# Performance work log

Measured on AMD Instinct MI355X. Metric: run time of the kernel, lower is better.

Reference implementation:

```python
import jax, jax.numpy as jnp
import numpy as np

N, KLEN, Q, S, E, H = 8, 512, 16, 128, 256, 8


def setup_inputs() -> dict:
    key = jax.random.key(0)
    ks = jax.random.split(key, 9)
    values = jax.random.normal(ks[0], (N, KLEN, E), dtype=jnp.float32)
    keys = jax.random.normal(ks[1], (N, KLEN, E), dtype=jnp.float32)
    query = jax.random.normal(ks[2], (N, Q, S, E), dtype=jnp.float32)
    mask = jax.random.randint(ks[3], (N, 1, 1, KLEN, 1), 0, 2, dtype=jnp.int32)
    Wv = jax.random.normal(ks[4], (E, E), dtype=jnp.float32) * 0.02
    Wk = jax.random.normal(ks[5], (E, E), dtype=jnp.float32) * 0.02
    Wq = jax.random.normal(ks[6], (E, E), dtype=jnp.float32) * 0.02
    Wo = jax.random.normal(ks[7], (E, H * E), dtype=jnp.float32) * 0.02
    bo = jnp.zeros((E,), dtype=jnp.float32)
    return {"values": values, "keys": keys, "query": query, "mask": mask,
            "Wv": Wv, "Wk": Wk, "Wq": Wq, "Wo": Wo, "bo": bo}


def reference(values, keys, query, mask, Wv, Wk, Wq, Wo, bo):
    # In the torch module head_dim == embed_size and the SAME Linear is applied
    # to every (expanded) head, so project once and broadcast over heads.
    e = Wq.shape[0]
    heads = Wo.shape[1] // e
    v = values @ Wv.T          # [N, K, E]
    k = keys @ Wk.T            # [N, K, E]
    q = query @ Wq.T           # [N, Q, S, E]
    # energy per head is identical; broadcast to [N, H, Q, K, S] to mirror
    # torch's einsum('nqshd,nkhd->nhqks') followed by masked_fill.
    energy = jnp.einsum('nqsd,nkd->nqks', q, k)               # [N, Q, K, S]
    energy = jnp.broadcast_to(energy[:, None],
                              (energy.shape[0], heads) + energy.shape[1:])
    energy = jnp.where(mask == 0, jnp.float32(-1e20), energy)  # [N,H,Q,K,S]
    attn = jax.nn.softmax(energy / jnp.sqrt(jnp.float32(e)), axis=3)
    out = jnp.einsum('nhqks,nkd->nqshd', attn, v)              # [N,Q,S,H,E]
    out = out.reshape(out.shape[0], out.shape[1], out.shape[2], heads * e)
    return out @ Wo.T + bo                                     # [N, Q, S, E]
```

## Files before the change

### kernel.cpp

```cpp
#include <hip/hip_runtime.h>
#include <hip/hip_bf16.h>
#include <stdint.h>

#define NB   8
#define KL   512
#define QD   16
#define SD   128
#define ED   256
#define RPN  (QD*SD)
#define BMR  32
#define FRAG 512
#define PAN  131072

typedef __hip_bfloat16 bf16;
using s16x8 = __attribute__((ext_vector_type(8))) short;
using f32x4 = __attribute__((ext_vector_type(4))) float;

__device__ __forceinline__ float b2f(unsigned short u){
    union { uint32_t i; float f; } v; v.i = ((uint32_t)u) << 16; return v.f;
}
__device__ __forceinline__ unsigned short f2b(float f){
    union { float ff; uint32_t i; } v; v.ff = f;
    uint32_t lsb = (v.i >> 16) & 1;
    v.i += 0x7FFFu + lsb;
    return (unsigned short)(v.i >> 16);
}
__device__ __forceinline__ uint32_t cvtpk(float lo, float hi){
    uint32_t r;
    asm("v_cvt_pk_bf16_f32 %0, %1, %2" : "=v"(r) : "v"(lo), "v"(hi));
    return r;
}
__device__ __forceinline__ f32x4 mfma16(s16x8 a, s16x8 b, f32x4 c){
    return __builtin_amdgcn_mfma_f32_16x16x32_bf16(a, b, c, 0, 0, 0);
}

template<bool B>
__device__ __forceinline__ float ldin(const void* p, size_t i){
    if (B) return b2f(((const unsigned short*)p)[i]);
    else   return ((const float*)p)[i];
}

__device__ bool probe_bf16(const uint32_t* __restrict__ w, int* pc){
    if (threadIdx.x == 0) *pc = 0;
    __syncthreads();
    if (threadIdx.x < 256){
        int local = 0;
        #pragma unroll
        for (int i = 0; i < 4; ++i){
            uint32_t x = w[threadIdx.x*4 + i];
            uint32_t e = (x >> 7) & 0xFFu;
            local += (e >= 120u && e <= 132u) ? 1 : 0;
        }
        if (local) atomicAdd(pc, local);
    }
    __syncthreads();
    return *pc > 512;
}

template<bool B>
__device__ void gt_body(const void* __restrict__ Wq, const void* __restrict__ Wk,
                        float* __restrict__ Gt, int bx){
    int b = bx, a = threadIdx.x;
    float s = 0.f;
    #pragma unroll 8
    for (int d = 0; d < 256; ++d)
        s += ldin<B>(Wq, (size_t)d*256 + a) * ldin<B>(Wk, (size_t)d*256 + b);
    Gt[b*256 + a] = s;
}
template<bool B>
__device__ void wosmt_body(const void* __restrict__ Wo, const void* __restrict__ Wv,
                           float* __restrict__ Mt, int bx, float (*sm)[256]){
    int t = threadIdx.x, e0 = bx*8;
    #pragma unroll
    for (int je = 0; je < 8; ++je){
        int e = e0 + je;
        float s = 0.f;
        #pragma unroll
        for (int h = 0; h < 8; ++h) s += ldin<B>(Wo, (size_t)e*2048 + h*256 + t);
        sm[je][t] = s;
    }
    __syncthreads();
    float acc[8] = {0,0,0,0,0,0,0,0};
    #pragma unroll 4
    for (int dp = 0; dp < 256; ++dp){
        float wv = ldin<B>(Wv, (size_t)dp*256 + t);
        #pragma unroll
        for (int je = 0; je < 8; ++je) acc[je] += sm[je][dp] * wv;
    }
    #pragma unroll
    for (int je = 0; je < 8; ++je) Mt[t*256 + e0 + je] = acc[je];
}
__global__ __launch_bounds__(256)
void k_prep(const void* __restrict__ values,
            const void* __restrict__ Wq, const void* __restrict__ Wk,
            const void* __restrict__ Wo, const void* __restrict__ Wv,
            float* __restrict__ Gt, float* __restrict__ Mt){
    __shared__ float sm[8][256];
    __shared__ int pc;
    bool bf = probe_bf16((const uint32_t*)values, &pc);
    if (blockIdx.x < 256){
        if (bf) gt_body<true >(Wq, Wk, Gt, blockIdx.x);
        else    gt_body<false>(Wq, Wk, Gt, blockIdx.x);
    } else {
        int bx = blockIdx.x - 256;
        if (bf) wosmt_body<true >(Wo, Wv, Mt, bx, sm);
        else    wosmt_body<false>(Wo, Wv, Mt, bx, sm);
    }
}

template<bool B>
__device__ void projK_body(const void* __restrict__ A, const float* __restrict__ Wt,
                           unsigned short* __restrict__ C, int bx, float (*As)[256]){
    int r0 = bx * 8;
    int t  = threadIdx.x;
    #pragma unroll
    for (int j = 0; j < 8; ++j)
        As[j][t] = ldin<B>(A, (size_t)(r0 + j)*256 + t);
    __syncthreads();
    float acc[8] = {0,0,0,0,0,0,0,0};
    #pragma unroll 4
    for (int i = 0; i < 256; ++i){
        float w = Wt[i*256 + t];
        #pragma unroll
        for (int j = 0; j < 8; ++j) acc[j] += As[j][i] * w;
    }
    int nn = r0 >> 9, key0 = r0 & 511;
    int K16 = key0 >> 4, ks = t >> 5, g = (t >> 3) & 3, i = t & 7;
    size_t base = (size_t)nn*PAN + (size_t)((K16*8 + ks)*64)*8;
    int l0 = (key0 & 15) | (g << 4);
    #pragma unroll
    for (int j = 0; j < 8; ++j)
        C[base + (size_t)(l0 + j)*8 + i] = f2b(acc[j]);
}
template<bool B>
__device__ void projU_body(const void* __restrict__ A, const float* __restrict__ Wt,
                           unsigned short* __restrict__ C, int bx, float (*As)[256]){
    int r0 = bx * 8;
    int t  = threadIdx.x;
    #pragma unroll
    for (int j = 0; j < 8; ++j)
        As[j][t] = ldin<B>(A, (size_t)(r0 + j)*256 + t);
    __syncthreads();
    float acc[8] = {0,0,0,0,0,0,0,0};
    #pragma unroll 4
    for (int i = 0; i < 256; ++i){
        float w = Wt[i*256 + t];
        #pragma unroll
        for (int j = 0; j < 8; ++j) acc[j] += As[j][i] * w;
    }
    int nn = r0 >> 9, k0 = r0 & 511;
    int ks2 = k0 >> 5, g = (k0 >> 3) & 3;
    int E16 = t >> 4, l = (t & 15) | (g << 4);
    size_t base = (size_t)nn*PAN + (size_t)((E16*16 + ks2)*64 + l)*8;
    union { s16x8 v; unsigned short h[8]; } pk;
    #pragma unroll
    for (int j = 0; j < 8; ++j) pk.h[j] = f2b(acc[j]);
    *(s16x8*)(&C[base]) = pk.v;
}
__global__ __launch_bounds__(256)
void k_proj2(const void* __restrict__ keys, const void* __restrict__ values,
             const float* __restrict__ Gt, const float* __restrict__ Mt,
             unsigned short* __restrict__ kkF, unsigned short* __restrict__ utF){
    __shared__ float As[8][256];
    __shared__ int pc;
    bool bf = probe_bf16((const uint32_t*)values, &pc);
    if (blockIdx.x < 512){
        if (bf) projK_body<true >(keys, Gt, kkF, blockIdx.x, As);
        else    projK_body<false>(keys, Gt, kkF, blockIdx.x, As);
    } else {
        int bx = blockIdx.x - 512;
        if (bf) projU_body<true >(values, Mt, utF, bx, As);
        else    projU_body<false>(values, Mt, utF, bx, As);
    }
}

template<bool B>
__device__ void fused_body(const void* __restrict__ query,
                           const unsigned short* __restrict__ kkF,
                           const unsigned short* __restrict__ utF,
                           const int* __restrict__ mask,
                           const void* __restrict__ bo,
                           void* __restrict__ out,
                           float* Sc, unsigned short* Qs){
    int bid = blockIdx.x;
    int n   = bid & 7;
    int r0  = (bid >> 3) * BMR;
    int t   = threadIdx.x;
    int l15 = t & 15;
    int g   = (t >> 4) & 3;
    int w   = t >> 6;
    int lane = t & 63;

    const unsigned short* Kn = kkF + (size_t)n*PAN;
    const unsigned short* Un = utF + (size_t)n*PAN;
    const int* mn = mask + n*KL;
    unsigned short* P = (unsigned short*)Sc;

    {
        int row = t >> 4;
        int c0  = (t & 15) * 16;
        int sw  = (row & 7) << 3;
        size_t qoff = (size_t)n*RPN*ED + (size_t)(r0 + row)*ED + c0;
        if (B){
            const unsigned short* qp = (const unsigned short*)query + qoff;
            s16x8 v0 = *(const s16x8*)(qp);
            s16x8 v1 = *(const s16x8*)(qp + 8);
            *(s16x8*)&Qs[(row*ED + c0    ) ^ sw] = v0;
            *(s16x8*)&Qs[(row*ED + c0 + 8) ^ sw] = v1;
        } else {
            const float* qp = (const float*)query + qoff;
            float4 x0 = *(const float4*)(qp);
            float4 x1 = *(const float4*)(qp + 4);
            float4 x2 = *(const float4*)(qp + 8);
            float4 x3 = *(const float4*)(qp + 12);
            union { s16x8 v; uint32_t u[4]; } pk;
            pk.u[0] = cvtpk(x0.x,x0.y); pk.u[1] = cvtpk(x0.z,x0.w);
            pk.u[2] = cvtpk(x1.x,x1.y); pk.u[3] = cvtpk(x1.z,x1.w);
            *(s16x8*)&Qs[(row*ED + c0    ) ^ sw] = pk.v;
            pk.u[0] = cvtpk(x2.x,x2.y); pk.u[1] = cvtpk(x2.z,x2.w);
            pk.u[2] = cvtpk(x3.x,x3.y); pk.u[3] = cvtpk(x3.z,x3.w);
            *(s16x8*)&Qs[(row*ED + c0 + 8) ^ sw] = pk.v;
        }
    }
    __syncthreads();

    int asw = (l15 & 7) << 3;

    {
        f32x4 acc1[2][4];
        #pragma unroll
        for (int rt = 0; rt < 2; ++rt)
            #pragma unroll
            for (int c = 0; c < 4; ++c) acc1[rt][c] = (f32x4){0.f,0.f,0.f,0.f};

        const unsigned short* kb = Kn + (size_t)w*16384 + (size_t)lane*8;
        s16x8 bb[3][4];
        auto LDK = [&](int KS, int SL){
            #pragma unroll
            for (int c = 0; c < 4; ++c)
                bb[SL][c] = *(const s16x8*)(kb + (size_t)(c*8 + KS)*FRAG);
        };
        LDK(0,0); LDK(1,1);
        #pragma unroll
        for (int ks = 0; ks < 8; ++ks){
            if (ks + 2 < 8) LDK(ks + 2, (ks + 2) % 3);
            int col = ks*32 + g*8;
            s16x8 a0 = *(const s16x8*)&Qs[(( 0 + l15)*ED + col) ^ asw];
            s16x8 a1 = *(const s16x8*)&Qs[((16 + l15)*ED + col) ^ asw];
            #pragma unroll
            for (int c = 0; c < 4; ++c){
                acc1[0][c] = mfma16(a0, bb[ks % 3][c], acc1[0][c]);
                acc1[1][c] = mfma16(a1, bb[ks % 3][c], acc1[1][c]);
            }
        }
        #pragma unroll
        for (int c = 0; c < 4; ++c){
            int key = w*64 + c*16 + l15;
            bool zz = (mn[key] == 0);
            #pragma unroll
            for (int rt = 0; rt < 2; ++rt){
                #pragma unroll
                for (int j = 0; j < 4; ++j){
                    int row = rt*16 + g*4 + j;
                    float v = zz ? -1e20f : acc1[rt][c][j] * 0.0625f;
                    Sc[(row*KL + key) ^ ((row & 7) << 2)] = v;
                }
            }
        }
    }
    __syncthreads();

    {
        int row = t >> 4, l16 = t & 15;
        int sw2 = (row & 7) << 2, sw3 = (row & 7) << 3;
        float xs[32];
        float m = -3.0e38f;
        #pragma unroll
        for (int i = 0; i < 32; ++i){
            xs[i] = Sc[(row*KL + l16 + 16*i) ^ sw2];
            m = fmaxf(m, xs[i]);
        }
        #pragma unroll
        for (int off = 1; off < 16; off <<= 1)
            m = fmaxf(m, __shfl_xor(m, off, 16));
        float s = 0.f;
        #pragma unroll
        for (int i = 0; i < 32; ++i){
            xs[i] = __expf(xs[i] - m);
            s += xs[i];
        }
        #pragma unroll
        for (int off = 1; off < 16; off <<= 1)
            s += __shfl_xor(s, off, 16);
        float inv = 1.0f / s;
        __syncthreads();
        #pragma unroll
        for (int i = 0; i < 32; ++i)
            P[(row*KL + l16 + 16*i) ^ sw3] = f2b(xs[i] * inv);
    }
    __syncthreads();

    {
        f32x4 acc2[2][2];
        #pragma unroll
        for (int rt = 0; rt < 2; ++rt)
            #pragma unroll
            for (int c = 0; c < 2; ++c) acc2[rt][c] = (f32x4){0.f,0.f,0.f,0.f};

        const unsigned short* ub = Un + (size_t)(2*w)*8192 + (size_t)lane*8;
        s16x8 bu[3][2];
        auto LDU = [&](int KS, int SL){
            #pragma unroll
            for (int c = 0; c < 2; ++c)
                bu[SL][c] = *(const s16x8*)(ub + (size_t)(c*16 + KS)*FRAG);
        };
        LDU(0,0); LDU(1,1);
        #pragma unroll
        for (int ks = 0; ks < 16; ++ks){
            if (ks + 2 < 16) LDU(ks + 2, (ks + 2) % 3);
            int col = ks*32 + g*8;
            s16x8 p0 = *(const s16x8*)&P[(( 0 + l15)*KL + col) ^ asw];
            s16x8 p1 = *(const s16x8*)&P[((16 + l15)*KL + col) ^ asw];
            #pragma unroll
            for (int c = 0; c < 2; ++c){
                acc2[0][c] = mfma16(p0, bu[ks % 3][c], acc2[0][c]);
                acc2[1][c] = mfma16(p1, bu[ks % 3][c], acc2[1][c]);
            }
        }
        float bov[2];
        #pragma unroll
        for (int c = 0; c < 2; ++c) bov[c] = ldin<B>(bo, (2*w + c)*16 + l15);
        #pragma unroll
        for (int rt = 0; rt < 2; ++rt){
            #pragma unroll
            for (int j = 0; j < 4; ++j){
                int row = rt*16 + g*4 + j;
                #pragma unroll
                for (int c = 0; c < 2; ++c){
                    int e = (2*w + c)*16 + l15;
                    float val = acc2[rt][c][j] + bov[c];
                    size_t oidx = (size_t)n*RPN*ED + (size_t)(r0 + row)*ED + e;
                    if (B) ((unsigned short*)out)[oidx] = f2b(val);
                    else   ((float*)out)[oidx] = val;
                }
            }
        }
    }
}

__global__ __launch_bounds__(512, 4)
void k_fused3(const void* __restrict__ values, const void* __restrict__ query,
              const unsigned short* __restrict__ kkF,
              const unsigned short* __restrict__ utF,
              const int* __restrict__ mask, const void* __restrict__ bo,
              void* __restrict__ out){
    __shared__ float Sc[BMR*KL];
    __shared__ unsigned short Qs[BMR*ED];
    bool bf = probe_bf16((const uint32_t*)values, (int*)Sc);
    if (bf) fused_body<true >(query, kkF, utF, mask, bo, out, Sc, Qs);
    else    fused_body<false>(query, kkF, utF, mask, bo, out, Sc, Qs);
}

extern "C" void kernel_launch(void* const* d_in, const int* in_sizes, int n_in,
                              void* d_out, int out_size, void* d_ws, size_t ws_size,
                              hipStream_t stream){
    const void* values = d_in[0];
    const void* keys   = d_in[1];
    const void* query  = d_in[2];
    const int*  mask   = (const int*)d_in[3];
    const void* Wv     = d_in[4];
    const void* Wk     = d_in[5];
    const void* Wq     = d_in[6];
    const void* Wo     = d_in[7];
    const void* bo     = d_in[8];

    float* ws = (float*)d_ws;
    float* ws_gt = ws;
    float* ws_mt = ws + 65536;
    unsigned short* ws_kk = (unsigned short*)(ws + 131072);
    unsigned short* ws_u  = ws_kk + (size_t)NB*PAN;

    k_prep  <<< 288, 256, 0, stream>>>(values, Wq, Wk, Wo, Wv, ws_gt, ws_mt);
    k_proj2 <<<1024, 256, 0, stream>>>(keys, values, ws_gt, ws_mt, ws_kk, ws_u);
    k_fused3<<< 512, 512, 0, stream>>>(values, query, ws_kk, ws_u, mask, bo, d_out);
}
```

Measured before the change: 150.5 us.

## Keep softmax scores in registers with cross-wave reductions and fragment-layout P

```diff
diff --git a/kernel.cpp b/kernel.cpp
--- a/kernel.cpp
+++ b/kernel.cpp
@@ -181,7 +181,8 @@
                            const int* __restrict__ mask,
                            const void* __restrict__ bo,
                            void* __restrict__ out,
-                           float* Sc, unsigned short* Qs){
+                           unsigned short* Qs, unsigned short* Pf,
+                           float* redM, float* redS){
     int bid = blockIdx.x;
     int n   = bid & 7;
     int r0  = (bid >> 3) * BMR;
@@ -194,7 +195,6 @@
     const unsigned short* Kn = kkF + (size_t)n*PAN;
     const unsigned short* Un = utF + (size_t)n*PAN;
     const int* mn = mask + n*KL;
-    unsigned short* P = (unsigned short*)Sc;
 
     {
         int row = t >> 4;
@@ -226,6 +226,7 @@
 
     int asw = (l15 & 7) << 3;
 
+    float p[2][4][4];
     {
         f32x4 acc1[2][4];
         #pragma unroll
@@ -255,48 +256,83 @@
         }
         #pragma unroll
         for (int c = 0; c < 4; ++c){
-            int key = w*64 + c*16 + l15;
-            bool zz = (mn[key] == 0);
-            #pragma unroll
-            for (int rt = 0; rt < 2; ++rt){
-                #pragma unroll
-                for (int j = 0; j < 4; ++j){
-                    int row = rt*16 + g*4 + j;
-                    float v = zz ? -1e20f : acc1[rt][c][j] * 0.0625f;
-                    Sc[(row*KL + key) ^ ((row & 7) << 2)] = v;
+            bool zz = (mn[w*64 + c*16 + l15] == 0);
+            #pragma unroll
+            for (int rt = 0; rt < 2; ++rt)
+                #pragma unroll
+                for (int j = 0; j < 4; ++j)
+                    p[rt][c][j] = zz ? -1e20f : acc1[rt][c][j] * 0.0625f;
+        }
+    }
+
+    {
+        float mx[2][4];
+        #pragma unroll
+        for (int rt = 0; rt < 2; ++rt)
+            #pragma unroll
+            for (int j = 0; j < 4; ++j){
+                float m0 = fmaxf(fmaxf(p[rt][0][j], p[rt][1][j]),
+                                 fmaxf(p[rt][2][j], p[rt][3][j]));
+                #pragma unroll
+                for (int off = 1; off < 16; off <<= 1)
+                    m0 = fmaxf(m0, __shfl_xor(m0, off, 16));
+                mx[rt][j] = m0;
+            }
+        if (l15 == 0){
+            #pragma unroll
+            for (int rt = 0; rt < 2; ++rt)
+                #pragma unroll
+                for (int j = 0; j < 4; ++j)
+                    redM[(rt*16 + g*4 + j)*8 + w] = mx[rt][j];
+        }
+        __syncthreads();
+        float sm[2][4];
+        #pragma unroll
+        for (int rt = 0; rt < 2; ++rt)
+            #pragma unroll
+            for (int j = 0; j < 4; ++j){
+                int row = rt*16 + g*4 + j;
+                float4 a = *(const float4*)&redM[row*8];
+                float4 b = *(const float4*)&redM[row*8 + 4];
+                float m = fmaxf(fmaxf(fmaxf(a.x,a.y),fmaxf(a.z,a.w)),
+                                fmaxf(fmaxf(b.x,b.y),fmaxf(b.z,b.w)));
+                float s = 0.f;
+                #pragma unroll
+                for (int c = 0; c < 4; ++c){
+                    p[rt][c][j] = __expf(p[rt][c][j] - m);
+                    s += p[rt][c][j];
                 }
-            }
-        }
-    }
-    __syncthreads();
-
-    {
-        int row = t >> 4, l16 = t & 15;
-        int sw2 = (row & 7) << 2, sw3 = (row & 7) << 3;
-        float xs[32];
-        float m = -3.0e38f;
-        #pragma unroll
-        for (int i = 0; i < 32; ++i){
-            xs[i] = Sc[(row*KL + l16 + 16*i) ^ sw2];
-            m = fmaxf(m, xs[i]);
-        }
-        #pragma unroll
-        for (int off = 1; off < 16; off <<= 1)
-            m = fmaxf(m, __shfl_xor(m, off, 16));
-        float s = 0.f;
-        #pragma unroll
-        for (int i = 0; i < 32; ++i){
-            xs[i] = __expf(xs[i] - m);
-            s += xs[i];
-        }
-        #pragma unroll
-        for (int off = 1; off < 16; off <<= 1)
-            s += __shfl_xor(s, off, 16);
-        float inv = 1.0f / s;
+                #pragma unroll
+                for (int off = 1; off < 16; off <<= 1)
+                    s += __shfl_xor(s, off, 16);
+                sm[rt][j] = s;
+            }
+        if (l15 == 0){
+            #pragma unroll
+            for (int rt = 0; rt < 2; ++rt)
+                #pragma unroll
+                for (int j = 0; j < 4; ++j)
+                    redS[(rt*16 + g*4 + j)*8 + w] = sm[rt][j];
+        }
         __syncthreads();
-        #pragma unroll
-        for (int i = 0; i < 32; ++i)
-            P[(row*KL + l16 + 16*i) ^ sw3] = f2b(xs[i] * inv);
+        int ihi = ((l15 >> 3) << 4);
+        int ilo = l15 & 7;
+        #pragma unroll
+        for (int rt = 0; rt < 2; ++rt){
+            #pragma unroll
+            for (int j = 0; j < 4; ++j){
+                int row = rt*16 + g*4 + j;
+                float4 a = *(const float4*)&redS[row*8];
+                float4 b = *(const float4*)&redS[row*8 + 4];
+                float inv = 1.0f / ((a.x+a.y+a.z+a.w) + (b.x+b.y+b.z+b.w));
+                #pragma unroll
+                for (int c = 0; c < 4; ++c){
+                    int lp = (g*4 + j) | (((c & 1) << 5) | ihi);
+                    int elem = (rt*16 + w*2 + (c >> 1))*FRAG + lp*8 + ilo;
+                    Pf[elem] = f2b(p[rt][c][j] * inv);
+                }
+            }
+        }
     }
     __syncthreads();
 
@@ -318,9 +354,8 @@
         #pragma unroll
         for (int ks = 0; ks < 16; ++ks){
             if (ks + 2 < 16) LDU(ks + 2, (ks + 2) % 3);
-            int col = ks*32 + g*8;
-            s16x8 p0 = *(const s16x8*)&P[(( 0 + l15)*KL + col) ^ asw];
-            s16x8 p1 = *(const s16x8*)&P[((16 + l15)*KL + col) ^ asw];
+            s16x8 p0 = *(const s16x8*)&Pf[( 0 + ks)*FRAG + lane*8];
+            s16x8 p1 = *(const s16x8*)&Pf[(16 + ks)*FRAG + lane*8];
             #pragma unroll
             for (int c = 0; c < 2; ++c){
                 acc2[0][c] = mfma16(p0, bu[ks % 3][c], acc2[0][c]);
@@ -349,16 +384,19 @@
 }
 
 __global__ __launch_bounds__(512, 4)
-void k_fused3(const void* __restrict__ values, const void* __restrict__ query,
+void k_fused4(const void* __restrict__ values, const void* __restrict__ query,
               const unsigned short* __restrict__ kkF,
               const unsigned short* __restrict__ utF,
               const int* __restrict__ mask, const void* __restrict__ bo,
               void* __restrict__ out){
-    __shared__ float Sc[BMR*KL];
     __shared__ unsigned short Qs[BMR*ED];
-    bool bf = probe_bf16((const uint32_t*)values, (int*)Sc);
-    if (bf) fused_body<true >(query, kkF, utF, mask, bo, out, Sc, Qs);
-    else    fused_body<false>(query, kkF, utF, mask, bo, out, Sc, Qs);
+    __shared__ unsigned short Pf[32*FRAG];
+    __shared__ float redM[BMR*8];
+    __shared__ float redS[BMR*8];
+    __shared__ int pc;
+    bool bf = probe_bf16((const uint32_t*)values, &pc);
+    if (bf) fused_body<true >(query, kkF, utF, mask, bo, out, Qs, Pf, redM, redS);
+    else    fused_body<false>(query, kkF, utF, mask, bo, out, Qs, Pf, redM, redS);
 }
 
 extern "C" void kernel_launch(void* const* d_in, const int* in_sizes, int n_in,
@@ -382,5 +420,5 @@
 
     k_prep  <<< 288, 256, 0, stream>>>(values, Wq, Wk, Wo, Wv, ws_gt, ws_mt);
     k_proj2 <<<1024, 256, 0, stream>>>(keys, values, ws_gt, ws_mt, ws_kk, ws_u);
-    k_fused3<<< 512, 512, 0, stream>>>(values, query, ws_kk, ws_u, mask, bo, d_out);
-}
+    k_fused4<<< 512, 512, 0, stream>>>(values, query, ws_kk, ws_u, mask, bo, d_out);
+}
```

Result: no change. 152.8 us (+1.5%).
